# Kernel optimization log

Measured on AMD Instinct MI355X. Metric: run time of the kernel, lower is better.

Reference implementation:

```python
import jax, jax.numpy as jnp
import numpy as np

B, L, C = 8, 2048, 512
CI = C // 2  # internal_units


def setup_inputs() -> dict:
    key = jax.random.key(0)
    ks = jax.random.split(key, 4)
    inputs = jax.random.normal(ks[0], (B, L, C), dtype=jnp.float32)
    # Conv1D kernel_size=1 == per-position linear; kernel_initializer='random_normal' (stddev 0.05)
    Wx = 0.05 * jax.random.normal(ks[1], (C, CI), dtype=jnp.float32)
    Wy = 0.05 * jax.random.normal(ks[2], (C, CI), dtype=jnp.float32)
    Wo = 0.05 * jax.random.normal(ks[3], (C, C), dtype=jnp.float32)
    bx = jnp.zeros((CI,), dtype=jnp.float32)
    by = jnp.zeros((CI,), dtype=jnp.float32)
    bo = jnp.zeros((C,), dtype=jnp.float32)
    return {"inputs": inputs, "Wx": Wx, "bx": bx, "Wy": Wy, "by": by, "Wo": Wo, "bo": bo}


def reference(inputs, Wx, bx, Wy, by, Wo, bo):
    # 1x1 conv projections (per-position linear layers with bias)
    x_proj = jnp.einsum('blc,ci->bli', inputs, Wx) + bx   # [B, L, Ci]
    y_proj = jnp.einsum('blc,ci->bli', inputs, Wy) + by   # [B, L, Ci]
    o_proj = jnp.einsum('blc,cd->bld', inputs, Wo) + bo   # [B, L, C]
    # scores: batched matmul x @ y^T -> [B, L, L]
    scores = jnp.einsum('bli,bmi->blm', x_proj, y_proj)
    # NOTE: softmax over axis=0 (the BATCH axis), as in the original module
    attn = jax.nn.softmax(scores, axis=0)
    s_dot = jnp.einsum('blm,bmc->blc', attn, o_proj)       # [B, L, C]
    return inputs + s_dot
```

## Files before the change

kernel.cpp:

```cpp
#include <hip/hip_runtime.h>


#define NB 8
#define NL 2048
#define NC 512
#define NCI 256

using f16x8 = __attribute__((ext_vector_type(8))) _Float16;
using f32x4 = __attribute__((ext_vector_type(4))) float;
typedef unsigned short u16;

__device__ __forceinline__ u16 f16b(float x) {
    _Float16 h = (_Float16)x;
    return __builtin_bit_cast(u16, h);
}
__device__ __forceinline__ float f16tof(u16 u) {
    return (float)__builtin_bit_cast(_Float16, u);
}
__device__ __forceinline__ void gload16(const void* g, void* l) {
    __builtin_amdgcn_global_load_lds((__attribute__((address_space(1))) void*)g,
                                     (__attribute__((address_space(3))) void*)l,
                                     16, 0, 0);
}

__global__ __launch_bounds__(256) void cvt_x_kernel(const float* __restrict__ X,
                                                    u16* __restrict__ Xf)
{
    size_t i = (size_t)blockIdx.x * 256 + threadIdx.x;
    const float4* X4 = (const float4*)X;
    float4 a = X4[2 * i], b = X4[2 * i + 1];
    u16 o[8] = {f16b(a.x), f16b(a.y), f16b(a.z), f16b(a.w),
                f16b(b.x), f16b(b.y), f16b(b.z), f16b(b.w)};
    ((uint4*)Xf)[i] = *(const uint4*)o;
}

__global__ __launch_bounds__(256) void cvt_w_kernel(
    const float* __restrict__ Wx, const float* __restrict__ Wy, const float* __restrict__ Wo,
    u16* __restrict__ WxT, u16* __restrict__ WyT, u16* __restrict__ WoT)
{
    const int bid = blockIdx.x, t = threadIdx.x;
#pragma unroll
    for (int kk = 0; kk < 2; ++kk) {
        const int k = t + kk * 256;
        if (bid < 256)      WxT[(size_t)bid * NC + k] = f16b(Wx[(size_t)k * NCI + bid]);
        else if (bid < 512) WyT[(size_t)(bid - 256) * NC + k] = f16b(Wy[(size_t)k * NCI + (bid - 256)]);
        else                WoT[(size_t)(bid - 512) * NC + k] = f16b(Wo[(size_t)k * NC + (bid - 512)]);
    }
}

__global__ __launch_bounds__(256) void proj_kernel(
    const u16* __restrict__ Xf,
    const u16* __restrict__ WxT, const u16* __restrict__ WyT, const u16* __restrict__ WoT,
    const float* __restrict__ bx, const float* __restrict__ by, const float* __restrict__ bo,
    u16* __restrict__ xp, u16* __restrict__ yp, u16* __restrict__ opT)
{
    __shared__ __align__(16) u16 SM[17408];
    u16* As = SM;
    u16* Bs = SM + 8192;

    const int tid = threadIdx.x;
    const int w = tid >> 6, lane = tid & 63;
    const int row0 = blockIdx.x * 128;
    const int cb = blockIdx.y;

    const u16* W; const float* bias; int n0, path;
    if (cb < 2)      { path = 0; n0 = cb * 128;       W = WxT; bias = bx; }
    else if (cb < 4) { path = 1; n0 = (cb - 2) * 128; W = WyT; bias = by; }
    else             { path = 2; n0 = (cb - 4) * 128; W = WoT; bias = bo; }

    f32x4 acc[4][4] = {};
    const int wm = (w & 1) * 64, wn = (w >> 1) * 64;
    const int fr = lane & 15, fq = lane >> 4;

    for (int k0 = 0; k0 < NC; k0 += 64) {
#pragma unroll
        for (int pass = 0; pass < 4; ++pass) {
            const int cbase = pass * 256 + w * 64;
            const int chunk = cbase + lane;
            const int r = chunk >> 3;
            const int kc = (chunk & 7) ^ (r & 7);
            gload16(Xf + (size_t)(row0 + r) * NC + k0 + kc * 8, (char*)As + cbase * 16);
            gload16(W  + (size_t)(n0  + r) * NC + k0 + kc * 8, (char*)Bs + cbase * 16);
        }
        __syncthreads();
        f16x8 a[4][2], b[4][2];
#pragma unroll
        for (int mi = 0; mi < 4; ++mi)
#pragma unroll
            for (int kt = 0; kt < 2; ++kt)
                a[mi][kt] = *(const f16x8*)&As[(wm + mi * 16 + fr) * 64 + ((kt * 4 + fq) ^ (fr & 7)) * 8];
#pragma unroll
        for (int ni = 0; ni < 4; ++ni)
#pragma unroll
            for (int kt = 0; kt < 2; ++kt)
                b[ni][kt] = *(const f16x8*)&Bs[(wn + ni * 16 + fr) * 64 + ((kt * 4 + fq) ^ (fr & 7)) * 8];
#pragma unroll
        for (int kt = 0; kt < 2; ++kt)
#pragma unroll
            for (int mi = 0; mi < 4; ++mi)
#pragma unroll
                for (int ni = 0; ni < 4; ++ni)
                    acc[mi][ni] = __builtin_amdgcn_mfma_f32_16x16x32_f16(a[mi][kt], b[ni][kt], acc[mi][ni], 0, 0, 0);
        __syncthreads();
    }

    if (path != 2) {
        u16* O = (path == 0) ? xp : yp;
#pragma unroll
        for (int mi = 0; mi < 4; ++mi) {
            const int grow = row0 + wm + mi * 16 + fq * 4;
#pragma unroll
            for (int ni = 0; ni < 4; ++ni) {
                const int gcol = n0 + wn + ni * 16 + fr;
                const float bv = bias[gcol];
#pragma unroll
                for (int r = 0; r < 4; ++r)
                    O[(size_t)(grow + r) * NCI + gcol] = f16b(acc[mi][ni][r] + bv);
            }
        }
    } else {
        u16* Ts = SM;
#pragma unroll
        for (int mi = 0; mi < 4; ++mi) {
            const int mb = wm + mi * 16 + fq * 4;
#pragma unroll
            for (int ni = 0; ni < 4; ++ni) {
                const int nl_ = wn + ni * 16 + fr;
                const float bv = bias[n0 + nl_];
#pragma unroll
                for (int r = 0; r < 4; ++r)
                    Ts[nl_ * 136 + mb + r] = f16b(acc[mi][ni][r] + bv);
            }
        }
        __syncthreads();
        const int b = row0 >> 11, m0 = row0 & 2047;
        u16* dst = opT + (size_t)b * NC * NL + (size_t)n0 * NL + m0;
        for (int i = tid; i < 128 * 16; i += 256) {
            const int c = i >> 4, ch = i & 15;
            uint4 v = *(const uint4*)&Ts[c * 136 + ch * 8];
            *(uint4*)&dst[(size_t)c * NL + ch * 8] = v;
        }
    }
}

__global__ __launch_bounds__(256) void score_softmax_kernel(
    const u16* __restrict__ xp, const u16* __restrict__ yp, u16* __restrict__ ATT)
{
    __shared__ __align__(16) u16 As[8192], Bs[8192];
    const int tid = threadIdx.x;
    const int w = tid >> 6, lane = tid & 63;
    const int row0 = blockIdx.x * 64, col0 = blockIdx.y * 64;
    const int wn = w * 16;
    const int fr = lane & 15, fq = lane >> 4;

    unsigned sv[NB][8];

#pragma unroll
    for (int b = 0; b < NB; ++b) {
        const u16* A = xp + (size_t)b * NL * NCI;
        const u16* B = yp + (size_t)b * NL * NCI;
        f32x4 acc[4] = {};
#pragma unroll
        for (int h = 0; h < 2; ++h) {
            const int k0 = h * 128;
#pragma unroll
            for (int pass = 0; pass < 4; ++pass) {
                const int cbase = pass * 256 + w * 64;
                const int chunk = cbase + lane;
                const int kh = chunk >> 9;
                const int r = (chunk >> 3) & 63;
                const int jj = (chunk & 7) ^ (r & 7);
                gload16(A + (size_t)(row0 + r) * NCI + k0 + kh * 64 + jj * 8, (char*)As + chunk * 16);
                gload16(B + (size_t)(col0 + r) * NCI + k0 + kh * 64 + jj * 8, (char*)Bs + chunk * 16);
            }
            __syncthreads();
#pragma unroll
            for (int kq = 0; kq < 4; ++kq) {
                const int rb = (kq >> 1) * 64;
                const int c = (((kq & 1) * 4 + fq) ^ (fr & 7)) * 8;
                f16x8 af[4], bf;
                bf = *(const f16x8*)&Bs[(rb + wn + fr) * 64 + c];
#pragma unroll
                for (int mi = 0; mi < 4; ++mi)
                    af[mi] = *(const f16x8*)&As[(rb + mi * 16 + fr) * 64 + c];
#pragma unroll
                for (int mi = 0; mi < 4; ++mi)
                    acc[mi] = __builtin_amdgcn_mfma_f32_16x16x32_f16(af[mi], bf, acc[mi], 0, 0, 0);
            }
            __syncthreads();
        }
#pragma unroll
        for (int mi = 0; mi < 4; ++mi) {
            sv[b][mi * 2 + 0] = (unsigned)f16b(acc[mi][0]) | ((unsigned)f16b(acc[mi][1]) << 16);
            sv[b][mi * 2 + 1] = (unsigned)f16b(acc[mi][2]) | ((unsigned)f16b(acc[mi][3]) << 16);
        }
    }

    const int gc = col0 + wn + fr;
#pragma unroll
    for (int mi = 0; mi < 4; ++mi) {
#pragma unroll
        for (int rp = 0; rp < 2; ++rp) {
            float v0[NB], v1[NB];
#pragma unroll
            for (int b = 0; b < NB; ++b) {
                unsigned u = sv[b][mi * 2 + rp];
                v0[b] = f16tof((u16)(u & 0xFFFF));
                v1[b] = f16tof((u16)(u >> 16));
            }
            float m0 = v0[0], m1 = v1[0];
#pragma unroll
            for (int b = 1; b < NB; ++b) { m0 = fmaxf(m0, v0[b]); m1 = fmaxf(m1, v1[b]); }
            float s0 = 0.f, s1 = 0.f;
#pragma unroll
            for (int b = 0; b < NB; ++b) {
                v0[b] = __expf(v0[b] - m0); s0 += v0[b];
                v1[b] = __expf(v1[b] - m1); s1 += v1[b];
            }
            const float i0 = 1.f / s0, i1 = 1.f / s1;
            const int gr0 = row0 + mi * 16 + fq * 4 + rp * 2;
#pragma unroll
            for (int b = 0; b < NB; ++b) {
                u16* dst = ATT + (size_t)b * NL * NL;
                dst[(size_t)gr0 * NL + gc]       = f16b(v0[b] * i0);
                dst[(size_t)(gr0 + 1) * NL + gc] = f16b(v1[b] * i1);
            }
        }
    }
}

__global__ __launch_bounds__(512) void out_kernel(
    const u16* __restrict__ ATT, const u16* __restrict__ opT,
    const float* __restrict__ X, float* __restrict__ Out)
{
    __shared__ __align__(16) u16 As[2][8192], Bs[2][8192];
    const int tid = threadIdx.x;
    const int w = tid >> 6, lane = tid & 63;

    const int id  = blockIdx.x + 16 * (blockIdx.y + 4 * blockIdx.z);
    const int nid = (id & 7) * 64 + (id >> 3);
    const int bx  = nid & 15;
    const int by  = (nid >> 4) & 3;
    const int b   = nid >> 6;

    const int row0 = bx * 128, col0 = by * 128;
    const u16* Aatt = ATT + (size_t)b * NL * NL;
    const u16* Bsrc = opT + (size_t)b * NC * NL;

    f32x4 acc[4][2] = {};
    const int wm = (w & 1) * 64, wn = (w >> 1) * 32;
    const int fr = lane & 15, fq = lane >> 4;

    auto stage = [&](int k0, int bu) {
#pragma unroll
        for (int pass = 0; pass < 2; ++pass) {
            const int cbase = pass * 512 + w * 64;
            const int chunk = cbase + lane;
            const int r = chunk >> 3;
            const int kc = (chunk & 7) ^ (r & 7);
            gload16(Aatt + (size_t)(row0 + r) * NL + k0 + kc * 8, (char*)&As[bu][0] + cbase * 16);
            gload16(Bsrc + (size_t)(col0 + r) * NL + k0 + kc * 8, (char*)&Bs[bu][0] + cbase * 16);
        }
    };

    stage(0, 0);
    int bu = 0;
    for (int it = 0; it < NL / 64; ++it) {
        __syncthreads();
        if (it + 1 < NL / 64) stage((it + 1) * 64, bu ^ 1);
        f16x8 af[4][2], bf[2][2];
#pragma unroll
        for (int mi = 0; mi < 4; ++mi)
#pragma unroll
            for (int kt = 0; kt < 2; ++kt)
                af[mi][kt] = *(const f16x8*)&As[bu][(wm + mi * 16 + fr) * 64 + ((kt * 4 + fq) ^ (fr & 7)) * 8];
#pragma unroll
        for (int ni = 0; ni < 2; ++ni)
#pragma unroll
            for (int kt = 0; kt < 2; ++kt)
                bf[ni][kt] = *(const f16x8*)&Bs[bu][(wn + ni * 16 + fr) * 64 + ((kt * 4 + fq) ^ (fr & 7)) * 8];
#pragma unroll
        for (int kt = 0; kt < 2; ++kt)
#pragma unroll
            for (int mi = 0; mi < 4; ++mi)
#pragma unroll
                for (int ni = 0; ni < 2; ++ni)
                    acc[mi][ni] = __builtin_amdgcn_mfma_f32_16x16x32_f16(af[mi][kt], bf[ni][kt], acc[mi][ni], 0, 0, 0);
        bu ^= 1;
    }
    const size_t ob = (size_t)b * NL * NC;
#pragma unroll
    for (int mi = 0; mi < 4; ++mi) {
        const int gr = row0 + wm + mi * 16 + fq * 4;
#pragma unroll
        for (int ni = 0; ni < 2; ++ni) {
            const int gc = col0 + wn + ni * 16 + fr;
#pragma unroll
            for (int r = 0; r < 4; ++r) {
                const size_t o = ob + (size_t)(gr + r) * NC + gc;
                Out[o] = X[o] + acc[mi][ni][r];
            }
        }
    }
}

extern "C" void kernel_launch(void* const* d_in, const int* in_sizes, int n_in,
                              void* d_out, int out_size, void* d_ws, size_t ws_size,
                              hipStream_t stream)
{
    const float* X  = (const float*)d_in[0];
    const float* Wx = (const float*)d_in[1];
    const float* bx = (const float*)d_in[2];
    const float* Wy = (const float*)d_in[3];
    const float* by = (const float*)d_in[4];
    const float* Wo = (const float*)d_in[5];
    const float* bo = (const float*)d_in[6];
    float* out = (float*)d_out;

    char* ws = (char*)d_ws;
    u16* ATT = (u16*)ws;
    u16* Xf  = (u16*)ws;
    char* p = ws + 67108864;
    u16* xp  = (u16*)p; p += 8388608;
    u16* yp  = (u16*)p; p += 8388608;
    u16* opT = (u16*)p; p += 16777216;
    u16* WxT = (u16*)p; p += 262144;
    u16* WyT = (u16*)p; p += 262144;
    u16* WoT = (u16*)p; p += 524288;

    cvt_x_kernel<<<4096, 256, 0, stream>>>(X, Xf);
    cvt_w_kernel<<<1024, 256, 0, stream>>>(Wx, Wy, Wo, WxT, WyT, WoT);
    proj_kernel<<<dim3(128, 8), 256, 0, stream>>>(Xf, WxT, WyT, WoT, bx, by, bo, xp, yp, opT);
    score_softmax_kernel<<<dim3(32, 32), 256, 0, stream>>>(xp, yp, ATT);
    out_kernel<<<dim3(16, 4, NB), 512, 0, stream>>>(ATT, opT, X, out);
}
```

Before: 201.4 us.

## Parallelize score kernel across batches per wave and softmax via LDS transpose

The score-softmax kernel now launches 512 threads, with each group of four waves computing a different batch at the same time (two batch groups of four). K is staged in 64-wide chunks for all four batches at once. Scores are then scattered into shared memory in a batch-interleaved layout so that each thread reads all 8 batch values for one (row, col) with a single 16-byte load. It then does the batch-axis softmax and writes coalesced rows of ATT. The aim is more parallelism per block and better-coalesced attention stores, at the cost of about 66KB of LDS and more barriers.

Measured after the change: 208.2 us. 1.03x slower.

```diff
diff --git a/kernel.cpp b/kernel.cpp
--- a/kernel.cpp
+++ b/kernel.cpp
@@ -143,89 +143,100 @@
     }
 }
 
-__global__ __launch_bounds__(256) void score_softmax_kernel(
+__global__ __launch_bounds__(512, 4) void score_softmax_kernel(
     const u16* __restrict__ xp, const u16* __restrict__ yp, u16* __restrict__ ATT)
 {
-    __shared__ __align__(16) u16 As[8192], Bs[8192];
+    __shared__ __align__(16) u16 SM[33280];
     const int tid = threadIdx.x;
     const int w = tid >> 6, lane = tid & 63;
     const int row0 = blockIdx.x * 64, col0 = blockIdx.y * 64;
-    const int wn = w * 16;
+    const int bb = w & 3, nh = w >> 2;
     const int fr = lane & 15, fq = lane >> 4;
 
-    unsigned sv[NB][8];
-
-#pragma unroll
-    for (int b = 0; b < NB; ++b) {
-        const u16* A = xp + (size_t)b * NL * NCI;
-        const u16* B = yp + (size_t)b * NL * NCI;
-        f32x4 acc[4] = {};
-#pragma unroll
-        for (int h = 0; h < 2; ++h) {
-            const int k0 = h * 128;
-#pragma unroll
-            for (int pass = 0; pass < 4; ++pass) {
-                const int cbase = pass * 256 + w * 64;
-                const int chunk = cbase + lane;
-                const int kh = chunk >> 9;
-                const int r = (chunk >> 3) & 63;
-                const int jj = (chunk & 7) ^ (r & 7);
-                gload16(A + (size_t)(row0 + r) * NCI + k0 + kh * 64 + jj * 8, (char*)As + chunk * 16);
-                gload16(B + (size_t)(col0 + r) * NCI + k0 + kh * 64 + jj * 8, (char*)Bs + chunk * 16);
+    const int rs = (tid >> 3) & 63;
+    const int jj = (tid & 7) ^ (rs & 7);
+
+    unsigned sv[2][16];
+
+#pragma unroll
+    for (int g = 0; g < 2; ++g) {
+        f32x4 acc[4][2] = {};
+#pragma unroll
+        for (int s = 0; s < 4; ++s) {
+            const int k0 = s * 64;
+#pragma unroll
+            for (int pass = 0; pass < 8; ++pass) {
+                const int ab = pass >> 2, b2 = pass & 3;
+                const u16* src = (ab ? yp : xp)
+                    + (size_t)(g * 4 + b2) * NL * NCI
+                    + (size_t)((ab ? col0 : row0) + rs) * NCI + k0 + jj * 8;
+                gload16(src, (char*)SM + pass * 8192 + tid * 16);
             }
             __syncthreads();
 #pragma unroll
-            for (int kq = 0; kq < 4; ++kq) {
-                const int rb = (kq >> 1) * 64;
-                const int c = (((kq & 1) * 4 + fq) ^ (fr & 7)) * 8;
-                f16x8 af[4], bf;
-                bf = *(const f16x8*)&Bs[(rb + wn + fr) * 64 + c];
+            for (int kt = 0; kt < 2; ++kt) {
+                const int coff = ((kt * 4 + fq) ^ (fr & 7)) * 8;
+                f16x8 af[4], bf[2];
 #pragma unroll
                 for (int mi = 0; mi < 4; ++mi)
-                    af[mi] = *(const f16x8*)&As[(rb + mi * 16 + fr) * 64 + c];
+                    af[mi] = *(const f16x8*)&SM[bb * 4096 + (mi * 16 + fr) * 64 + coff];
+#pragma unroll
+                for (int ni = 0; ni < 2; ++ni)
+                    bf[ni] = *(const f16x8*)&SM[16384 + bb * 4096 + (nh * 32 + ni * 16 + fr) * 64 + coff];
 #pragma unroll
                 for (int mi = 0; mi < 4; ++mi)
-                    acc[mi] = __builtin_amdgcn_mfma_f32_16x16x32_f16(af[mi], bf, acc[mi], 0, 0, 0);
+#pragma unroll
+                    for (int ni = 0; ni < 2; ++ni)
+                        acc[mi][ni] = __builtin_amdgcn_mfma_f32_16x16x32_f16(af[mi], bf[ni], acc[mi][ni], 0, 0, 0);
             }
             __syncthreads();
         }
 #pragma unroll
-        for (int mi = 0; mi < 4; ++mi) {
-            sv[b][mi * 2 + 0] = (unsigned)f16b(acc[mi][0]) | ((unsigned)f16b(acc[mi][1]) << 16);
-            sv[b][mi * 2 + 1] = (unsigned)f16b(acc[mi][2]) | ((unsigned)f16b(acc[mi][3]) << 16);
-        }
-    }
-
-    const int gc = col0 + wn + fr;
-#pragma unroll
-    for (int mi = 0; mi < 4; ++mi) {
-#pragma unroll
-        for (int rp = 0; rp < 2; ++rp) {
-            float v0[NB], v1[NB];
-#pragma unroll
-            for (int b = 0; b < NB; ++b) {
-                unsigned u = sv[b][mi * 2 + rp];
-                v0[b] = f16tof((u16)(u & 0xFFFF));
-                v1[b] = f16tof((u16)(u >> 16));
-            }
-            float m0 = v0[0], m1 = v1[0];
-#pragma unroll
-            for (int b = 1; b < NB; ++b) { m0 = fmaxf(m0, v0[b]); m1 = fmaxf(m1, v1[b]); }
-            float s0 = 0.f, s1 = 0.f;
-#pragma unroll
-            for (int b = 0; b < NB; ++b) {
-                v0[b] = __expf(v0[b] - m0); s0 += v0[b];
-                v1[b] = __expf(v1[b] - m1); s1 += v1[b];
-            }
-            const float i0 = 1.f / s0, i1 = 1.f / s1;
-            const int gr0 = row0 + mi * 16 + fq * 4 + rp * 2;
-#pragma unroll
-            for (int b = 0; b < NB; ++b) {
-                u16* dst = ATT + (size_t)b * NL * NL;
-                dst[(size_t)gr0 * NL + gc]       = f16b(v0[b] * i0);
-                dst[(size_t)(gr0 + 1) * NL + gc] = f16b(v1[b] * i1);
-            }
-        }
+        for (int mi = 0; mi < 4; ++mi)
+#pragma unroll
+            for (int ni = 0; ni < 2; ++ni) {
+                sv[g][mi * 4 + ni * 2 + 0] = (unsigned)f16b(acc[mi][ni][0]) | ((unsigned)f16b(acc[mi][ni][1]) << 16);
+                sv[g][mi * 4 + ni * 2 + 1] = (unsigned)f16b(acc[mi][ni][2]) | ((unsigned)f16b(acc[mi][ni][3]) << 16);
+            }
+    }
+
+#pragma unroll
+    for (int g = 0; g < 2; ++g)
+#pragma unroll
+        for (int mi = 0; mi < 4; ++mi)
+#pragma unroll
+            for (int ni = 0; ni < 2; ++ni)
+#pragma unroll
+                for (int rp = 0; rp < 2; ++rp) {
+                    const unsigned u = sv[g][mi * 4 + ni * 2 + rp];
+                    const int r_ = mi * 16 + fq * 4 + rp * 2;
+                    const int c_ = nh * 32 + ni * 16 + fr;
+                    SM[(r_ * 65 + c_) * 8 + g * 4 + bb]         = (u16)(u & 0xFFFF);
+                    SM[((r_ + 1) * 65 + c_) * 8 + g * 4 + bb]   = (u16)(u >> 16);
+                }
+    __syncthreads();
+
+#pragma unroll
+    for (int j = 0; j < 8; ++j) {
+        const int row = j * 8 + w;
+        const int col = lane;
+        const uint4 v = *(const uint4*)&SM[(row * 65 + col) * 8];
+        float f[NB];
+        f[0] = f16tof((u16)(v.x & 0xFFFF)); f[1] = f16tof((u16)(v.x >> 16));
+        f[2] = f16tof((u16)(v.y & 0xFFFF)); f[3] = f16tof((u16)(v.y >> 16));
+        f[4] = f16tof((u16)(v.z & 0xFFFF)); f[5] = f16tof((u16)(v.z >> 16));
+        f[6] = f16tof((u16)(v.w & 0xFFFF)); f[7] = f16tof((u16)(v.w >> 16));
+        float m = f[0];
+#pragma unroll
+        for (int b = 1; b < NB; ++b) m = fmaxf(m, f[b]);
+        float ssum = 0.f;
+#pragma unroll
+        for (int b = 0; b < NB; ++b) { f[b] = __expf(f[b] - m); ssum += f[b]; }
+        const float inv = 1.f / ssum;
+        const size_t go = (size_t)(row0 + row) * NL + col0 + col;
+#pragma unroll
+        for (int b = 0; b < NB; ++b)
+            ATT[(size_t)b * NL * NL + go] = f16b(f[b] * inv);
     }
 }
 
@@ -331,6 +342,6 @@
     cvt_x_kernel<<<4096, 256, 0, stream>>>(X, Xf);
     cvt_w_kernel<<<1024, 256, 0, stream>>>(Wx, Wy, Wo, WxT, WyT, WoT);
     proj_kernel<<<dim3(128, 8), 256, 0, stream>>>(Xf, WxT, WyT, WoT, bx, by, bo, xp, yp, opT);
-    score_softmax_kernel<<<dim3(32, 32), 256, 0, stream>>>(xp, yp, ATT);
+    score_softmax_kernel<<<dim3(32, 32), 512, 0, stream>>>(xp, yp, ATT);
     out_kernel<<<dim3(16, 4, NB), 512, 0, stream>>>(ATT, opT, X, out);
 }
```
